# Optimization experiments

Measured on AMD Instinct MI355X. Metric: run time of the kernel, lower is better.

## Reference

```python
import jax, jax.numpy as jnp
import numpy as np

V = 100000   # num_regular_embeddings (full vocab)
K = 20000    # num custom (Poincare) embeddings
P = 300      # custom embedding dim
E = 256      # regular / output embedding dim
B = 1024
L = 256


def logmap0(v):
    # project from Poincare ball (c=1) to tangent space at origin
    norm = jnp.linalg.norm(v, axis=-1, keepdims=True)
    safe = jnp.where(norm > 0, norm, 0.5)            # avoid 0/0 and arctanh(0)/0
    scale = jnp.where(norm > 0, jnp.arctanh(safe) / safe, 1.0)
    return scale * v


def mobius_add(x, y):
    x2 = jnp.sum(x * x, axis=-1, keepdims=True)
    y2 = jnp.sum(y * y, axis=-1, keepdims=True)
    xy = jnp.sum(x * y, axis=-1, keepdims=True)
    num = (1 + 2 * xy + y2) * x + (1 - x2) * y
    denom = jnp.maximum(1 + 2 * xy + x2 * y2, 1e-15)
    return num / denom


def setup_inputs() -> dict:
    key = jax.random.key(0)
    k_x, k_perm, k_cw, k_rw, k_lw = jax.random.split(key, 5)

    x = jax.random.randint(k_x, (B, L), 0, V, dtype=jnp.int32)

    # K distinct custom vocab indices, excluding 0 (padding)
    custom_indices = jax.random.permutation(k_perm, jnp.arange(1, V, dtype=jnp.int32))[:K]

    # vocab -> custom table index (1..K), 0 for non-custom
    vocab_to_custom = jnp.zeros((V,), dtype=jnp.int32).at[custom_indices].set(
        jnp.arange(1, K + 1, dtype=jnp.int32))
    # vocab -> regular table index (0..V-K-1) for non-custom slots
    regular_vocab = jnp.where(vocab_to_custom == 0)[0]  # concrete, size V-K
    vocab_to_regular = jnp.zeros((V,), dtype=jnp.int32).at[regular_vocab].set(
        jnp.arange(V - K, dtype=jnp.int32))

    # fixed (pretrained, frozen) custom weights inside unit ball; row 0 = padding
    custom_fixed_w = (jax.random.normal(k_cw, (K + 1, P), dtype=jnp.float32) * 0.02).at[0].set(0.0)
    # trainable custom table initialized to zeros (as in the module)
    custom_train_w = jnp.zeros((K + 1, P), dtype=jnp.float32)
    # regular embedding table, row 0 = padding
    regular_w = (jax.random.normal(k_rw, (V - K, E), dtype=jnp.float32) * 0.02).at[0].set(0.0)
    # linear transform P -> E
    lin_w = jax.random.normal(k_lw, (E, P), dtype=jnp.float32) * 0.05
    lin_b = jnp.zeros((E,), dtype=jnp.float32)

    return {"x": x, "custom_indices": custom_indices,
            "vocab_to_custom": vocab_to_custom, "vocab_to_regular": vocab_to_regular,
            "custom_fixed_w": custom_fixed_w, "custom_train_w": custom_train_w,
            "regular_w": regular_w, "lin_w": lin_w, "lin_b": lin_b}


def reference(x, custom_indices, vocab_to_custom, vocab_to_regular,
              custom_fixed_w, custom_train_w, regular_w, lin_w, lin_b):
    mask = jnp.isin(x, custom_indices)                     # [B, L]
    custom_feat = jnp.where(mask, x, 0)
    regular_feat = jnp.where(mask, 0, x)

    cm = vocab_to_custom[custom_feat]                      # [B, L]
    fixed = logmap0(custom_fixed_w[cm])                    # [B, L, P]
    train = custom_train_w[cm]                             # [B, L, P]
    custom_emb = mobius_add(fixed, train)                  # [B, L, P]

    regular_emb = regular_w[vocab_to_regular[regular_feat]]  # [B, L, E]

    custom_emb = jnp.einsum("blp,ep->ble", custom_emb, lin_w) + lin_b
    return custom_emb + regular_emb
```

## Files before the change

### kernel.cpp

```cpp
#include <hip/hip_runtime.h>
#include <stdint.h>
#include <math.h>

#define NTOK (1024 * 256)
#define TPB  128
#define P_DIM 300
#define P_PAD 320
#define P_LDS 328
#define E_DIM 256

typedef __attribute__((ext_vector_type(8))) short bf16x8_t;
typedef __attribute__((ext_vector_type(4))) float f32x4_t;

__device__ __forceinline__ unsigned short f2b(float f) {
    union { float f; unsigned int i; } v; v.f = f;
    unsigned int x = v.i;
    return (unsigned short)((x + 0x7FFFu + ((x >> 16) & 1u)) >> 16);
}

__global__ __launch_bounds__(256) void k0_convert(
        const float* __restrict__ lin_w, unsigned short* __restrict__ lin_w_pad) {
    int idx = blockIdx.x * 256 + threadIdx.x;
    int e = idx / P_PAD;
    int k = idx - e * P_PAD;
    lin_w_pad[idx] = (k < P_DIM) ? f2b(lin_w[(size_t)e * P_DIM + k]) : (unsigned short)0;
}

__global__ __launch_bounds__(256) void k_fused(
        const int* __restrict__ x, const int* __restrict__ v2c,
        const int* __restrict__ v2r,
        const float* __restrict__ fixed_w,
        const float* __restrict__ train_w,
        const float* __restrict__ regular_w,
        const unsigned short* __restrict__ lin_w_pad,
        const float* __restrict__ lin_b,
        float* __restrict__ out) {
    __shared__ __align__(16) unsigned short semb[32][P_LDS];
    __shared__ int stok[TPB];
    __shared__ int scm[TPB];
    __shared__ int rinfo[TPB];
    __shared__ int s_n;

    int tid  = threadIdx.x;
    int wid  = tid >> 6;
    int lane = tid & 63;
    int base = blockIdx.x * TPB;

    if (tid == 0) s_n = 0;
    __syncthreads();

    if (tid < TPB) {
        int t  = base + tid;
        int xv = x[t];
        int cm = v2c[xv];
        int ri = -1;
        if (cm > 0) {
            int p = atomicAdd(&s_n, 1);
            stok[p] = t;
            scm[p]  = cm;
        } else {
            ri = v2r[xv];
        }
        rinfo[tid] = ri;
    }
    __syncthreads();
    int n = s_n;

    f32x4_t lb4 = *(const f32x4_t*)(lin_b + lane * 4);
    #pragma unroll 4
    for (int it = 0; it < TPB / 4; it++) {
        int li = wid * (TPB / 4) + it;
        int ri = rinfo[li];
        if (ri >= 0) {
            f32x4_t rf = *(const f32x4_t*)(regular_w + (size_t)ri * E_DIM + lane * 4);
            f32x4_t o = rf + lb4;
            __builtin_nontemporal_store(
                o, (f32x4_t*)(out + (size_t)(base + li) * E_DIM + lane * 4));
        }
    }

    if (n == 0) return;

    int col  = lane & 15;
    int kgrp = lane >> 4;
    int e0w  = wid * 64;
    int rbase = kgrp * 4;
    float lbe[4], rr0[4];
    int rid0 = v2r[0];
    const float* rrow0 = regular_w + (size_t)rid0 * E_DIM;
    #pragma unroll
    for (int nt = 0; nt < 4; nt++) {
        lbe[nt] = lin_b[e0w + nt * 16 + col];
        rr0[nt] = rrow0[e0w + nt * 16 + col];
    }

    for (int c0 = 0; c0 < n; c0 += 32) {
        int cn = n - c0; if (cn > 32) cn = 32;

        for (int i = wid; i < cn; i += 4) {
            int cm = scm[c0 + i];
            const float* fw = fixed_w + (size_t)cm * P_DIM;
            const float* tw = train_w + (size_t)cm * P_DIM;
            float w[5], tr[5];
            float sw2 = 0.f, st2 = 0.f, swt = 0.f;
            #pragma unroll
            for (int s = 0; s < 5; s++) {
                int j = lane + 64 * s;
                float wv = 0.f, tv = 0.f;
                if (j < P_DIM) { wv = fw[j]; tv = tw[j]; }
                w[s] = wv; tr[s] = tv;
                sw2 = fmaf(wv, wv, sw2); st2 = fmaf(tv, tv, st2); swt = fmaf(wv, tv, swt);
            }
            #pragma unroll
            for (int m = 32; m >= 1; m >>= 1) {
                sw2 += __shfl_xor(sw2, m, 64);
                st2 += __shfl_xor(st2, m, 64);
                swt += __shfl_xor(swt, m, 64);
            }
            float norm = sqrtf(sw2);
            norm = fminf(norm, 0.9999999f);
            float scale = (norm > 0.f) ? (atanhf(norm) / norm) : 1.0f;
            float x2 = scale * scale * sw2;
            float y2 = st2;
            float xy = scale * swt;
            float c1 = (1.f + 2.f * xy + y2) * scale;
            float c2 = (1.f - x2);
            float den = fmaxf(1.f + 2.f * xy + x2 * y2, 1e-15f);
            float inv = 1.f / den;
            #pragma unroll
            for (int s = 0; s < 5; s++) {
                int j = lane + 64 * s;
                float v = (j < P_DIM) ? (c1 * w[s] + c2 * tr[s]) * inv : 0.f;
                semb[i][j] = f2b(v);
            }
        }
        __syncthreads();

        f32x4_t acc[2][4];
        #pragma unroll
        for (int a = 0; a < 2; a++)
            #pragma unroll
            for (int b = 0; b < 4; b++) acc[a][b] = (f32x4_t)(0.f);

        #pragma unroll
        for (int kk = 0; kk < 10; kk++) {
            int k0 = kk * 32 + kgrp * 8;
            bf16x8_t afr[2], bfr[4];
            afr[0] = *(const bf16x8_t*)(&semb[col][k0]);
            afr[1] = *(const bf16x8_t*)(&semb[16 + col][k0]);
            #pragma unroll
            for (int nt = 0; nt < 4; nt++) {
                int e = e0w + nt * 16 + col;
                bfr[nt] = *(const bf16x8_t*)(lin_w_pad + (size_t)e * P_PAD + k0);
            }
            #pragma unroll
            for (int mt = 0; mt < 2; mt++)
                #pragma unroll
                for (int nt = 0; nt < 4; nt++)
                    acc[mt][nt] = __builtin_amdgcn_mfma_f32_16x16x32_bf16(
                        afr[mt], bfr[nt], acc[mt][nt], 0, 0, 0);
        }

        #pragma unroll
        for (int mt = 0; mt < 2; mt++) {
            #pragma unroll
            for (int r = 0; r < 4; r++) {
                int row = mt * 16 + rbase + r;
                if (row < cn) {
                    int t = stok[c0 + row];
                    float* orow = out + (size_t)t * E_DIM;
                    #pragma unroll
                    for (int nt = 0; nt < 4; nt++) {
                        __builtin_nontemporal_store(
                            acc[mt][nt][r] + lbe[nt] + rr0[nt],
                            orow + e0w + nt * 16 + col);
                    }
                }
            }
        }
        __syncthreads();
    }
}

extern "C" void kernel_launch(void* const* d_in, const int* in_sizes, int n_in,
                              void* d_out, int out_size, void* d_ws, size_t ws_size,
                              hipStream_t stream) {
    const int* x   = (const int*)d_in[0];
    const int* v2c = (const int*)d_in[2];
    const int* v2r = (const int*)d_in[3];
    const float* fixed_w   = (const float*)d_in[4];
    const float* train_w   = (const float*)d_in[5];
    const float* regular_w = (const float*)d_in[6];
    const float* lin_w     = (const float*)d_in[7];
    const float* lin_b     = (const float*)d_in[8];
    float* out = (float*)d_out;

    unsigned short* lin_w_pad = (unsigned short*)d_ws;

    k0_convert<<<(E_DIM * P_PAD) / 256, 256, 0, stream>>>(lin_w, lin_w_pad);
    k_fused<<<NTOK / TPB, 256, 0, stream>>>(x, v2c, v2r, fixed_w, train_w,
                                            regular_w, lin_w_pad, lin_b, out);
}
```

Before: 542.7 us.

## Split regular-row copy into its own kernel and fold weight conversion into it

Moves the regular-embedding gather and bias add into a separate streaming kernel that writes every token row unconditionally, processing 256 tokens per block with batched 8-row loads. The lin_w bf16 conversion is folded into the first blocks of that kernel, removing one launch. The custom kernel now only compacts custom tokens and runs the MFMA path, overwriting their rows afterward. Custom rows get written twice, which adds write traffic and relies on stream ordering between the two kernels.

```diff
diff --git a/kernel.cpp b/kernel.cpp
--- a/kernel.cpp
+++ b/kernel.cpp
@@ -3,7 +3,8 @@
 #include <math.h>
 
 #define NTOK (1024 * 256)
-#define TPB  128
+#define CPY_TOK 256
+#define CUS_TOK 128
 #define P_DIM 300
 #define P_PAD 320
 #define P_LDS 328
@@ -18,15 +19,48 @@
     return (unsigned short)((x + 0x7FFFu + ((x >> 16) & 1u)) >> 16);
 }
 
-__global__ __launch_bounds__(256) void k0_convert(
-        const float* __restrict__ lin_w, unsigned short* __restrict__ lin_w_pad) {
-    int idx = blockIdx.x * 256 + threadIdx.x;
-    int e = idx / P_PAD;
-    int k = idx - e * P_PAD;
-    lin_w_pad[idx] = (k < P_DIM) ? f2b(lin_w[(size_t)e * P_DIM + k]) : (unsigned short)0;
-}
-
-__global__ __launch_bounds__(256) void k_fused(
+__global__ __launch_bounds__(256) void kA_copy(
+        const int* __restrict__ x, const int* __restrict__ v2r,
+        const float* __restrict__ regular_w, const float* __restrict__ lin_b,
+        const float* __restrict__ lin_w, unsigned short* __restrict__ lin_w_pad,
+        float* __restrict__ out) {
+    int tid  = threadIdx.x;
+    int wid  = tid >> 6;
+    int lane = tid & 63;
+
+    if (blockIdx.x < (E_DIM * P_PAD) / 256) {
+        int idx = blockIdx.x * 256 + tid;
+        int e = idx / P_PAD;
+        int k = idx - e * P_PAD;
+        lin_w_pad[idx] = (k < P_DIM) ? f2b(lin_w[(size_t)e * P_DIM + k])
+                                     : (unsigned short)0;
+    }
+
+    int base = blockIdx.x * CPY_TOK + wid * 64;
+    int xv = x[base + lane];
+    int rv = v2r[xv];
+    f32x4_t lb4 = *(const f32x4_t*)(lin_b + lane * 4);
+
+    #pragma unroll 1
+    for (int it0 = 0; it0 < 64; it0 += 8) {
+        int ris[8];
+        f32x4_t rows[8];
+        #pragma unroll
+        for (int u = 0; u < 8; u++) ris[u] = __shfl(rv, it0 + u, 64);
+        #pragma unroll
+        for (int u = 0; u < 8; u++)
+            rows[u] = *(const f32x4_t*)(regular_w
+                        + (size_t)ris[u] * E_DIM + lane * 4);
+        #pragma unroll
+        for (int u = 0; u < 8; u++) {
+            f32x4_t o = rows[u] + lb4;
+            __builtin_nontemporal_store(
+                o, (f32x4_t*)(out + (size_t)(base + it0 + u) * E_DIM + lane * 4));
+        }
+    }
+}
+
+__global__ __launch_bounds__(256) void kB_custom(
         const int* __restrict__ x, const int* __restrict__ v2c,
         const int* __restrict__ v2r,
         const float* __restrict__ fixed_w,
@@ -36,54 +70,35 @@
         const float* __restrict__ lin_b,
         float* __restrict__ out) {
     __shared__ __align__(16) unsigned short semb[32][P_LDS];
-    __shared__ int stok[TPB];
-    __shared__ int scm[TPB];
-    __shared__ int rinfo[TPB];
+    __shared__ int stok[CUS_TOK];
+    __shared__ int scm[CUS_TOK];
     __shared__ int s_n;
 
     int tid  = threadIdx.x;
     int wid  = tid >> 6;
     int lane = tid & 63;
-    int base = blockIdx.x * TPB;
+    int base = blockIdx.x * CUS_TOK;
 
     if (tid == 0) s_n = 0;
     __syncthreads();
 
-    if (tid < TPB) {
+    if (tid < CUS_TOK) {
         int t  = base + tid;
         int xv = x[t];
         int cm = v2c[xv];
-        int ri = -1;
         if (cm > 0) {
             int p = atomicAdd(&s_n, 1);
             stok[p] = t;
             scm[p]  = cm;
-        } else {
-            ri = v2r[xv];
-        }
-        rinfo[tid] = ri;
+        }
     }
     __syncthreads();
     int n = s_n;
-
-    f32x4_t lb4 = *(const f32x4_t*)(lin_b + lane * 4);
-    #pragma unroll 4
-    for (int it = 0; it < TPB / 4; it++) {
-        int li = wid * (TPB / 4) + it;
-        int ri = rinfo[li];
-        if (ri >= 0) {
-            f32x4_t rf = *(const f32x4_t*)(regular_w + (size_t)ri * E_DIM + lane * 4);
-            f32x4_t o = rf + lb4;
-            __builtin_nontemporal_store(
-                o, (f32x4_t*)(out + (size_t)(base + li) * E_DIM + lane * 4));
-        }
-    }
-
     if (n == 0) return;
 
-    int col  = lane & 15;
-    int kgrp = lane >> 4;
-    int e0w  = wid * 64;
+    int col   = lane & 15;
+    int kgrp  = lane >> 4;
+    int e0w   = wid * 64;
     int rbase = kgrp * 4;
     float lbe[4], rr0[4];
     int rid0 = v2r[0];
@@ -197,7 +212,8 @@
 
     unsigned short* lin_w_pad = (unsigned short*)d_ws;
 
-    k0_convert<<<(E_DIM * P_PAD) / 256, 256, 0, stream>>>(lin_w, lin_w_pad);
-    k_fused<<<NTOK / TPB, 256, 0, stream>>>(x, v2c, v2r, fixed_w, train_w,
-                                            regular_w, lin_w_pad, lin_b, out);
-}
+    kA_copy<<<NTOK / CPY_TOK, 256, 0, stream>>>(x, v2r, regular_w, lin_b,
+                                                lin_w, lin_w_pad, out);
+    kB_custom<<<NTOK / CUS_TOK, 256, 0, stream>>>(x, v2c, v2r, fixed_w, train_w,
+                                                  regular_w, lin_w_pad, lin_b, out);
+}
```

Measured after the change: 507.8 us. 1.07x faster.
